# Performance work log

Measured on AMD Instinct MI355X. Metric: run time of the kernel, lower is better.

The kernel has to match this reference:

```python
import jax, jax.numpy as jnp
import numpy as np

N, IN_F, H, D = 3072, 512, 8, 64


def setup_inputs() -> dict:
    key = jax.random.key(0)
    k1, k2, k3, k4, k5 = jax.random.split(key, 5)
    x = jax.random.normal(k1, (N, IN_F), dtype=jnp.float32)
    adj = jax.random.randint(k2, (N, N), 0, 2, dtype=jnp.int32)
    # xavier-uniform-like scales
    s_W = (6.0 / (IN_F + H * D)) ** 0.5
    s_a = (6.0 / (H + D)) ** 0.5
    W = jax.random.uniform(k3, (H * D, IN_F), dtype=jnp.float32, minval=-s_W, maxval=s_W)
    a_src = jax.random.uniform(k4, (H, D), dtype=jnp.float32, minval=-s_a, maxval=s_a)
    a_dst = jax.random.uniform(k5, (H, D), dtype=jnp.float32, minval=-s_a, maxval=s_a)
    return {"x": x, "adj": adj, "W": W, "a_src": a_src, "a_dst": a_dst}


def reference(x, adj, W, a_src, a_dst):
    n = x.shape[0]
    Hh, d = a_src.shape
    h = (x @ W.T).reshape(n, Hh, d)                      # [n, H, d]
    e_src = jnp.einsum('nhd,hd->nh', h, a_src)           # [n, H]
    e_dst = jnp.einsum('nhd,hd->nh', h, a_dst)           # [n, H]
    e = e_src[:, None, :] + e_dst[None, :, :]            # [n, n, H], e[i,j]=src_i+dst_j
    e = jax.nn.leaky_relu(e, negative_slope=0.2)
    mask = (adj + jnp.eye(n, dtype=adj.dtype)) > 0       # [n, n]
    e = jnp.where(mask[:, :, None], e, -jnp.inf)
    alpha = jax.nn.softmax(e, axis=1)                    # softmax over j (neighbors)
    # out[i,h,d] = sum_j alpha[i,j,h] * h[j,h,d]  (dropout=0 / eval mode)
    out = jnp.einsum('ijh,jhd->ihd', alpha, h)
    return out.reshape(n, Hh * d)                        # concat=True
```

## Files before the change

### kernel.cpp

```cpp
#include <hip/hip_runtime.h>
#include <hip/hip_bf16.h>

typedef __bf16 bf16x8 __attribute__((ext_vector_type(8)));
typedef _Float16 half8 __attribute__((ext_vector_type(8)));
typedef _Float16 half2v __attribute__((ext_vector_type(2)));
typedef short s16x2 __attribute__((ext_vector_type(2)));
typedef float f32x4 __attribute__((ext_vector_type(4)));
typedef float f32x16 __attribute__((ext_vector_type(16)));

#define NROW 3072
#define NF 512
#define NH 8
#define ND 64
#define GEMM_BLOCKS 384

__device__ __forceinline__ unsigned gat_enc_key(float f) {
    unsigned u = __float_as_uint(f);
    return (f < 0.f) ? ~u : (u | 0x80000000u);
}
__device__ __forceinline__ float gat_dec_key(unsigned k) {
    unsigned u = (k & 0x80000000u) ? (k ^ 0x80000000u) : ~k;
    return __uint_as_float(u);
}

__device__ __forceinline__ bf16x8 gat_ld_cvt8(const float* p) {
    float4 f0 = *reinterpret_cast<const float4*>(p);
    float4 f1 = *reinterpret_cast<const float4*>(p + 4);
    bf16x8 o = { (__bf16)f0.x, (__bf16)f0.y, (__bf16)f0.z, (__bf16)f0.w,
                 (__bf16)f1.x, (__bf16)f1.y, (__bf16)f1.z, (__bf16)f1.w };
    return o;
}

__global__ __launch_bounds__(256) void gat_gemm_bp(const float* __restrict__ x,
                                                   const float* __restrict__ W,
                                                   _Float16* __restrict__ hT,
                                                   const int* __restrict__ adj,
                                                   unsigned long long* __restrict__ bits64,
                                                   const float* __restrict__ a_src,
                                                   const float* __restrict__ a_dst,
                                                   float* __restrict__ e_srcT,
                                                   float* __restrict__ e_dstT,
                                                   unsigned* __restrict__ maxkey) {
    __shared__ __align__(16) __bf16 sA[2][4096];
    __shared__ __align__(16) __bf16 sB[2][4096];
    __shared__ float ered[2][2][2][32];

    if (blockIdx.x >= GEMM_BLOCKS) {
        int i = blockIdx.x - GEMM_BLOCKS;
        int wave = threadIdx.x >> 6;
        int lane = threadIdx.x & 63;
        const int* row = adj + i * NROW;
#pragma unroll
        for (int it = 0; it < 12; ++it) {
            int base = wave * 768 + it * 64;
            int j = base + lane;
            bool pred = (row[j] > 0) || (j == i);
            unsigned long long bal = __ballot(pred);
            if (lane == 0) bits64[i * 48 + (base >> 6)] = bal;
        }
        return;
    }

    int b = blockIdx.x;
    int i0 = (b >> 3) * 64;
    int o0 = (b & 7) * 64;
    int head = b & 7;
    int tid = threadIdx.x;
    int wave = tid >> 6;
    int lane = tid & 63;
    int half = lane >> 5;
    int l31 = lane & 31;
    int wr = wave >> 1;
    int wc = wave & 1;

    int v0 = tid, v1 = tid + 256;
    int r0 = v0 >> 3, r1 = v1 >> 3;
    int cc0 = ((v0 & 7) ^ (r0 & 7)) << 3;
    int cc1 = ((v1 & 7) ^ (r1 & 7)) << 3;
    const float* gA0 = x + (i0 + r0) * NF + cc0;
    const float* gA1 = x + (i0 + r1) * NF + cc1;
    const float* gB0 = W + (o0 + r0) * NF + cc0;
    const float* gB1 = W + (o0 + r1) * NF + cc1;

    *reinterpret_cast<bf16x8*>(&sA[0][v0 * 8]) = gat_ld_cvt8(gA0);
    *reinterpret_cast<bf16x8*>(&sA[0][v1 * 8]) = gat_ld_cvt8(gA1);
    *reinterpret_cast<bf16x8*>(&sB[0][v0 * 8]) = gat_ld_cvt8(gB0);
    *reinterpret_cast<bf16x8*>(&sB[0][v1 * 8]) = gat_ld_cvt8(gB1);
    __syncthreads();

    f32x16 acc = {};
    int arow = (wr * 32 + l31) * 64;
    int brow = (wc * 32 + l31) * 64;
    int sw7 = l31 & 7;

    for (int c = 0; c < 8; ++c) {
        bf16x8 na0, na1, nb0, nb1;
        bool more = (c < 7);
        if (more) {
            na0 = gat_ld_cvt8(gA0 + (c + 1) * 64);
            na1 = gat_ld_cvt8(gA1 + (c + 1) * 64);
            nb0 = gat_ld_cvt8(gB0 + (c + 1) * 64);
            nb1 = gat_ld_cvt8(gB1 + (c + 1) * 64);
        }
        const __bf16* pa = &sA[c & 1][0];
        const __bf16* pb = &sB[c & 1][0];
#pragma unroll
        for (int ks = 0; ks < 4; ++ks) {
            int q = (((ks << 1) | half) ^ sw7) << 3;
            bf16x8 a = *reinterpret_cast<const bf16x8*>(pa + arow + q);
            bf16x8 bb = *reinterpret_cast<const bf16x8*>(pb + brow + q);
            acc = __builtin_amdgcn_mfma_f32_32x32x16_bf16(a, bb, acc, 0, 0, 0);
        }
        if (more) {
            *reinterpret_cast<bf16x8*>(&sA[(c + 1) & 1][v0 * 8]) = na0;
            *reinterpret_cast<bf16x8*>(&sA[(c + 1) & 1][v1 * 8]) = na1;
            *reinterpret_cast<bf16x8*>(&sB[(c + 1) & 1][v0 * 8]) = nb0;
            *reinterpret_cast<bf16x8*>(&sB[(c + 1) & 1][v1 * 8]) = nb1;
        }
        __syncthreads();
    }

    _Float16* tt = reinterpret_cast<_Float16*>(&sA[0][0]) + wave * 1280;
#pragma unroll
    for (int reg = 0; reg < 16; ++reg) {
        int rowl = (reg & 3) + 8 * (reg >> 2) + 4 * half;
        tt[rowl * 40 + l31] = (_Float16)acc[reg];
    }
    int orow = lane >> 1;
    int li = (lane & 1) * 16;
    half8 h0, h1;
#pragma unroll
    for (int t = 0; t < 8; ++t) h0[t] = tt[(li + t) * 40 + orow];
#pragma unroll
    for (int t = 0; t < 8; ++t) h1[t] = tt[(li + 8 + t) * 40 + orow];
    _Float16* op = hT + (long)(o0 + wc * 32 + orow) * NROW + i0 + wr * 32 + li;
    *reinterpret_cast<half8*>(op) = h0;
    *reinterpret_cast<half8*>(op + 8) = h1;

    half8 hv0 = *reinterpret_cast<const half8*>(tt + l31 * 40 + half * 16);
    half8 hv1 = *reinterpret_cast<const half8*>(tt + l31 * 40 + half * 16 + 8);
    const float* ap = a_src + head * ND + wc * 32 + half * 16;
    const float* dp = a_dst + head * ND + wc * 32 + half * 16;
    float4 as0 = *reinterpret_cast<const float4*>(ap);
    float4 as1 = *reinterpret_cast<const float4*>(ap + 4);
    float4 as2 = *reinterpret_cast<const float4*>(ap + 8);
    float4 as3 = *reinterpret_cast<const float4*>(ap + 12);
    float4 ad0 = *reinterpret_cast<const float4*>(dp);
    float4 ad1 = *reinterpret_cast<const float4*>(dp + 4);
    float4 ad2 = *reinterpret_cast<const float4*>(dp + 8);
    float4 ad3 = *reinterpret_cast<const float4*>(dp + 12);
    float ps = 0.f, pd = 0.f;
    ps += (float)hv0[0]*as0.x + (float)hv0[1]*as0.y + (float)hv0[2]*as0.z + (float)hv0[3]*as0.w;
    ps += (float)hv0[4]*as1.x + (float)hv0[5]*as1.y + (float)hv0[6]*as1.z + (float)hv0[7]*as1.w;
    ps += (float)hv1[0]*as2.x + (float)hv1[1]*as2.y + (float)hv1[2]*as2.z + (float)hv1[3]*as2.w;
    ps += (float)hv1[4]*as3.x + (float)hv1[5]*as3.y + (float)hv1[6]*as3.z + (float)hv1[7]*as3.w;
    pd += (float)hv0[0]*ad0.x + (float)hv0[1]*ad0.y + (float)hv0[2]*ad0.z + (float)hv0[3]*ad0.w;
    pd += (float)hv0[4]*ad1.x + (float)hv0[5]*ad1.y + (float)hv0[6]*ad1.z + (float)hv0[7]*ad1.w;
    pd += (float)hv1[0]*ad2.x + (float)hv1[1]*ad2.y + (float)hv1[2]*ad2.z + (float)hv1[3]*ad2.w;
    pd += (float)hv1[4]*ad3.x + (float)hv1[5]*ad3.y + (float)hv1[6]*ad3.z + (float)hv1[7]*ad3.w;
    ps += __shfl_xor(ps, 32, 64);
    pd += __shfl_xor(pd, 32, 64);
    if (half == 0) { ered[0][wr][wc][l31] = ps; ered[1][wr][wc][l31] = pd; }
    __syncthreads();
    if (wc == 0) {
        float pst = ered[0][wr][0][l31] + ered[0][wr][1][l31];
        float pdt = ered[1][wr][0][l31] + ered[1][wr][1][l31];
        if (half == 0) {
            e_srcT[head * NROW + i0 + wr * 32 + l31] = pst;
            e_dstT[head * NROW + i0 + wr * 32 + l31] = pdt;
        }
        float mx = pdt;
#pragma unroll
        for (int off = 1; off < 32; off <<= 1) mx = fmaxf(mx, __shfl_xor(mx, off, 64));
        if (lane == 0) atomicMax(&maxkey[head], gat_enc_key(mx));
    }
}

__global__ __launch_bounds__(256) void gat_attn(const unsigned* __restrict__ bits,
                                                const float* __restrict__ e_srcT,
                                                const float* __restrict__ e_dstT,
                                                const unsigned* __restrict__ maxkey,
                                                const _Float16* __restrict__ hT,
                                                _Float16* __restrict__ num,
                                                float* __restrict__ den) {
    constexpr int JCHUNK = NROW / 4;
    constexpr int NC = JCHUNK / 64;
    __shared__ unsigned lds_P[JCHUNK / 2];
    __shared__ unsigned lds_Q[JCHUNK / 2];
    __shared__ __align__(16) _Float16 hbuf[2][4096];
    int b = blockIdx.x;
    int head = b & 7;
    int jc = (b >> 3) & 3;
    int i0 = ((b >> 3) >> 2) * 128;
    int jbase = jc * JCHUNK;
    int tid = threadIdx.x;
    int wave = tid >> 6;
    int lane = tid & 63;
    int half = lane >> 5;
    int l31 = lane & 31;

    float Mg = gat_dec_key(maxkey[head]);
    for (int p = tid; p < JCHUNK / 2; p += 256) {
        float t0 = e_dstT[head * NROW + jbase + 2 * p] - Mg;
        float t1 = e_dstT[head * NROW + jbase + 2 * p + 1] - Mg;
        half2v P = { (_Float16)__expf(t0), (_Float16)__expf(t1) };
        half2v Q = { (_Float16)__expf(0.2f * t0), (_Float16)__expf(0.2f * t1) };
        lds_P[p] = __builtin_bit_cast(unsigned, P);
        lds_Q[p] = __builtin_bit_cast(unsigned, Q);
    }

    int irow = i0 + wave * 32 + l31;
    float u = e_srcT[head * NROW + irow] + Mg;
    float Rf = fminf(__expf(-0.8f * u), 60000.f);
    _Float16 Rh = (_Float16)Rf;
    half2v R2 = { Rh, Rh };
    const half8 ones8 = { (_Float16)1.f, (_Float16)1.f, (_Float16)1.f, (_Float16)1.f,
                          (_Float16)1.f, (_Float16)1.f, (_Float16)1.f, (_Float16)1.f };
    const unsigned* brow = bits + irow * 96 + jc * (JCHUNK / 32);

    int s0 = tid, s1 = tid + 256;
    const _Float16* gp0 = hT + (head * ND + ((s0 >> 6) & 1) * 32 + (s0 & 31)) * NROW
                             + jbase + (s0 >> 7) * 16 + ((s0 >> 5) & 1) * 8;
    const _Float16* gp1 = hT + (head * ND + ((s1 >> 6) & 1) * 32 + (s1 & 31)) * NROW
                             + jbase + (s1 >> 7) * 16 + ((s1 >> 5) & 1) * 8;
    *reinterpret_cast<half8*>(&hbuf[0][tid * 8])         = *reinterpret_cast<const half8*>(gp0);
    *reinterpret_cast<half8*>(&hbuf[0][(tid + 256) * 8]) = *reinterpret_cast<const half8*>(gp1);
    __syncthreads();

    f32x16 acc0 = {};
    f32x16 acc1 = {};
    f32x16 acc2 = {};
    uint2 wm = *reinterpret_cast<const uint2*>(brow);

    for (int k = 0; k < NC; ++k) {
        half8 st0, st1;
        uint2 wmn = wm;
        bool more = (k + 1 < NC);
        if (more) {
            st0 = *reinterpret_cast<const half8*>(gp0 + (k + 1) * 64);
            st1 = *reinterpret_cast<const half8*>(gp1 + (k + 1) * 64);
            wmn = *reinterpret_cast<const uint2*>(brow + (k + 1) * 2);
        }
        const _Float16* hb = &hbuf[k & 1][0];
#pragma unroll
        for (int js = 0; js < 4; ++js) {
            unsigned word = (js < 2) ? wm.x : wm.y;
            unsigned w8 = (word >> ((js & 1) * 16 + half * 8)) & 0xffu;
            unsigned long long S64 = ((unsigned long long)(w8 & 0x55u) << 15)
                                   | ((unsigned long long)(w8 & 0xAAu) << 30);
            uint4 Pv = *reinterpret_cast<const uint4*>(&lds_P[k * 32 + js * 8 + half * 4]);
            uint4 Qv = *reinterpret_cast<const uint4*>(&lds_Q[k * 32 + js * 8 + half * 4]);
            unsigned pr[4] = { Pv.x, Pv.y, Pv.z, Pv.w };
            unsigned qr[4] = { Qv.x, Qv.y, Qv.z, Qv.w };
            unsigned am[4];
#pragma unroll
            for (int t = 0; t < 4; ++t) {
                half2v qq = __builtin_bit_cast(half2v, qr[t]) * R2;
                half2v mx = __builtin_elementwise_max(
                                __builtin_bit_cast(half2v, pr[t]), qq);
                unsigned Wt = (unsigned)(S64 >> (2 * t));
                s16x2 mks = __builtin_bit_cast(s16x2, Wt) >> 15;
                am[t] = __builtin_bit_cast(unsigned, mx)
                      & __builtin_bit_cast(unsigned, mks);
            }
            uint4 m4 = { am[0], am[1], am[2], am[3] };
            half8 af = __builtin_bit_cast(half8, m4);
            half8 v0 = *reinterpret_cast<const half8*>(hb + (js * 128 + lane) * 8);
            half8 v1 = *reinterpret_cast<const half8*>(hb + (js * 128 + 64 + lane) * 8);
            acc0 = __builtin_amdgcn_mfma_f32_32x32x16_f16(af, v0, acc0, 0, 0, 0);
            acc1 = __builtin_amdgcn_mfma_f32_32x32x16_f16(af, v1, acc1, 0, 0, 0);
            acc2 = __builtin_amdgcn_mfma_f32_32x32x16_f16(af, ones8, acc2, 0, 0, 0);
        }
        if (more) {
            *reinterpret_cast<half8*>(&hbuf[(k + 1) & 1][tid * 8])         = st0;
            *reinterpret_cast<half8*>(&hbuf[(k + 1) & 1][(tid + 256) * 8]) = st1;
        }
        wm = wmn;
        __syncthreads();
    }

#pragma unroll
    for (int reg = 0; reg < 16; ++reg) {
        int rowl = (reg & 3) + 8 * (reg >> 2) + 4 * half;
        if (l31 == 0)
            den[(long)(jc * NROW + i0 + wave * 32 + rowl) * NH + head] = acc2[reg];
        long ob = (long)(jc * NROW + i0 + wave * 32 + rowl) * NF + head * ND + l31;
        num[ob]      = (_Float16)acc0[reg];
        num[ob + 32] = (_Float16)acc1[reg];
    }
}

__global__ __launch_bounds__(256) void gat_final(const _Float16* __restrict__ num,
                                                 const float* __restrict__ den,
                                                 float* __restrict__ out) {
    int idx = (blockIdx.x * 256 + threadIdx.x) * 8;
    int i = idx >> 9;
    int c = idx & 511;
    int head = c >> 6;
    half8 n0 = *reinterpret_cast<const half8*>(num + (long)i * NF + c);
    half8 n1 = *reinterpret_cast<const half8*>(num + (long)(NROW + i) * NF + c);
    half8 n2 = *reinterpret_cast<const half8*>(num + (long)(2 * NROW + i) * NF + c);
    half8 n3 = *reinterpret_cast<const half8*>(num + (long)(3 * NROW + i) * NF + c);
    float ds = den[i * NH + head] + den[(NROW + i) * NH + head]
             + den[(2 * NROW + i) * NH + head] + den[(3 * NROW + i) * NH + head];
    float inv = 1.0f / fmaxf(ds, 1e-30f);
    float r0 = ((float)n0[0] + (float)n1[0] + (float)n2[0] + (float)n3[0]) * inv;
    float r1 = ((float)n0[1] + (float)n1[1] + (float)n2[1] + (float)n3[1]) * inv;
    float r2 = ((float)n0[2] + (float)n1[2] + (float)n2[2] + (float)n3[2]) * inv;
    float r3 = ((float)n0[3] + (float)n1[3] + (float)n2[3] + (float)n3[3]) * inv;
    float r4 = ((float)n0[4] + (float)n1[4] + (float)n2[4] + (float)n3[4]) * inv;
    float r5 = ((float)n0[5] + (float)n1[5] + (float)n2[5] + (float)n3[5]) * inv;
    float r6 = ((float)n0[6] + (float)n1[6] + (float)n2[6] + (float)n3[6]) * inv;
    float r7 = ((float)n0[7] + (float)n1[7] + (float)n2[7] + (float)n3[7]) * inv;
    float4 o0 = { r0, r1, r2, r3 };
    float4 o1 = { r4, r5, r6, r7 };
    *reinterpret_cast<float4*>(out + idx)     = o0;
    *reinterpret_cast<float4*>(out + idx + 4) = o1;
}

extern "C" void kernel_launch(void* const* d_in, const int* in_sizes, int n_in,
                              void* d_out, int out_size, void* d_ws, size_t ws_size,
                              hipStream_t stream) {
    const float* x_raw  = (const float*)d_in[0];
    const int*   adj    = (const int*)d_in[1];
    const float* W_raw  = (const float*)d_in[2];
    const float* as_raw = (const float*)d_in[3];
    const float* ad_raw = (const float*)d_in[4];
    float* out = (float*)d_out;

    char* ws = (char*)d_ws;
    _Float16* hT     = (_Float16*)(ws);
    float*    e_srcT = (float*)(ws + 3145728);
    float*    e_dstT = (float*)(ws + 3244032);
    unsigned* maxkey = (unsigned*)(ws + 3342336);
    unsigned* bits   = (unsigned*)(ws + 3342400);
    _Float16* num    = (_Float16*)(ws + 8192064);
    float*    den    = (float*)(ws + 20774976);

    hipMemsetAsync(maxkey, 0, 64, stream);
    gat_gemm_bp<<<GEMM_BLOCKS + NROW, 256, 0, stream>>>(x_raw, W_raw, hT, adj,
                                                        (unsigned long long*)bits,
                                                        as_raw, ad_raw,
                                                        e_srcT, e_dstT, maxkey);
    gat_attn<<<24 * 4 * 8, 256, 0, stream>>>(bits, e_srcT, e_dstT, maxkey, hT, num, den);
    gat_final<<<NROW * NF / 2048, 256, 0, stream>>>(num, den, out);
}
```

Baseline: 143.3 us.

## Pack adjacency bits with vectorized int4 loads and shrink GEMM K-tile to 32

The adjacency bitmask pass now has each thread read 32 ints with int4 loads and build one 32-bit word, replacing per-element wave ballots over 3072 blocks with 1152 denser blocks. Bit order stays the same, so downstream consumers are unaffected. The projection GEMM switches from a 64-wide XOR-swizzled K tile to a 32-wide padded (stride 40) tile with 16 stages, which lowers shared memory use and per-thread loads. In exchange the GEMM pays more barriers per block.

```diff
diff --git a/kernel.cpp b/kernel.cpp
--- a/kernel.cpp
+++ b/kernel.cpp
@@ -13,6 +13,7 @@
 #define NH 8
 #define ND 64
 #define GEMM_BLOCKS 384
+#define BP_BLOCKS 1152
 
 __device__ __forceinline__ unsigned gat_enc_key(float f) {
     unsigned u = __float_as_uint(f);
@@ -35,29 +36,33 @@
                                                    const float* __restrict__ W,
                                                    _Float16* __restrict__ hT,
                                                    const int* __restrict__ adj,
-                                                   unsigned long long* __restrict__ bits64,
+                                                   unsigned* __restrict__ bits,
                                                    const float* __restrict__ a_src,
                                                    const float* __restrict__ a_dst,
                                                    float* __restrict__ e_srcT,
                                                    float* __restrict__ e_dstT,
                                                    unsigned* __restrict__ maxkey) {
-    __shared__ __align__(16) __bf16 sA[2][4096];
-    __shared__ __align__(16) __bf16 sB[2][4096];
+    __shared__ __align__(16) _Float16 smem[10240];
     __shared__ float ered[2][2][2][32];
 
     if (blockIdx.x >= GEMM_BLOCKS) {
-        int i = blockIdx.x - GEMM_BLOCKS;
-        int wave = threadIdx.x >> 6;
-        int lane = threadIdx.x & 63;
-        const int* row = adj + i * NROW;
-#pragma unroll
-        for (int it = 0; it < 12; ++it) {
-            int base = wave * 768 + it * 64;
-            int j = base + lane;
-            bool pred = (row[j] > 0) || (j == i);
-            unsigned long long bal = __ballot(pred);
-            if (lane == 0) bits64[i * 48 + (base >> 6)] = bal;
-        }
+        int g = (blockIdx.x - GEMM_BLOCKS) * 256 + threadIdx.x;
+        int row = g / 96;
+        int seg = g - row * 96;
+        const int* p = adj + row * NROW + seg * 32;
+        unsigned w = 0;
+#pragma unroll
+        for (int q = 0; q < 8; ++q) {
+            int4 v = *reinterpret_cast<const int4*>(p + q * 4);
+            unsigned b0 = (v.x > 0) ? 1u : 0u;
+            unsigned b1 = (v.y > 0) ? 2u : 0u;
+            unsigned b2 = (v.z > 0) ? 4u : 0u;
+            unsigned b3 = (v.w > 0) ? 8u : 0u;
+            w |= (b0 | b1 | b2 | b3) << (q * 4);
+        }
+        int d = row - seg * 32;
+        if ((unsigned)d < 32u) w |= 1u << d;
+        bits[g] = w;
         return;
     }
 
@@ -73,54 +78,47 @@
     int wr = wave >> 1;
     int wc = wave & 1;
 
-    int v0 = tid, v1 = tid + 256;
-    int r0 = v0 >> 3, r1 = v1 >> 3;
-    int cc0 = ((v0 & 7) ^ (r0 & 7)) << 3;
-    int cc1 = ((v1 & 7) ^ (r1 & 7)) << 3;
-    const float* gA0 = x + (i0 + r0) * NF + cc0;
-    const float* gA1 = x + (i0 + r1) * NF + cc1;
-    const float* gB0 = W + (o0 + r0) * NF + cc0;
-    const float* gB1 = W + (o0 + r1) * NF + cc1;
-
-    *reinterpret_cast<bf16x8*>(&sA[0][v0 * 8]) = gat_ld_cvt8(gA0);
-    *reinterpret_cast<bf16x8*>(&sA[0][v1 * 8]) = gat_ld_cvt8(gA1);
-    *reinterpret_cast<bf16x8*>(&sB[0][v0 * 8]) = gat_ld_cvt8(gB0);
-    *reinterpret_cast<bf16x8*>(&sB[0][v1 * 8]) = gat_ld_cvt8(gB1);
+    __bf16* sA = reinterpret_cast<__bf16*>(smem);
+    __bf16* sB = reinterpret_cast<__bf16*>(smem) + 5120;
+
+    int r = tid >> 2;
+    int pp = tid & 3;
+    const float* gA = x + (i0 + r) * NF + pp * 8;
+    const float* gB = W + (o0 + r) * NF + pp * 8;
+    int dslot = r * 40 + pp * 8;
+
+    *reinterpret_cast<bf16x8*>(sA + dslot) = gat_ld_cvt8(gA);
+    *reinterpret_cast<bf16x8*>(sB + dslot) = gat_ld_cvt8(gB);
     __syncthreads();
 
     f32x16 acc = {};
-    int arow = (wr * 32 + l31) * 64;
-    int brow = (wc * 32 + l31) * 64;
-    int sw7 = l31 & 7;
-
-    for (int c = 0; c < 8; ++c) {
-        bf16x8 na0, na1, nb0, nb1;
-        bool more = (c < 7);
+    int arow = (wr * 32 + l31) * 40;
+    int brow = (wc * 32 + l31) * 40;
+
+    for (int c = 0; c < 16; ++c) {
+        bf16x8 na, nb;
+        bool more = (c < 15);
         if (more) {
-            na0 = gat_ld_cvt8(gA0 + (c + 1) * 64);
-            na1 = gat_ld_cvt8(gA1 + (c + 1) * 64);
-            nb0 = gat_ld_cvt8(gB0 + (c + 1) * 64);
-            nb1 = gat_ld_cvt8(gB1 + (c + 1) * 64);
-        }
-        const __bf16* pa = &sA[c & 1][0];
-        const __bf16* pb = &sB[c & 1][0];
-#pragma unroll
-        for (int ks = 0; ks < 4; ++ks) {
-            int q = (((ks << 1) | half) ^ sw7) << 3;
+            na = gat_ld_cvt8(gA + (c + 1) * 32);
+            nb = gat_ld_cvt8(gB + (c + 1) * 32);
+        }
+        const __bf16* pa = sA + (c & 1) * 2560;
+        const __bf16* pb = sB + (c & 1) * 2560;
+#pragma unroll
+        for (int ks = 0; ks < 2; ++ks) {
+            int q = (((ks << 1) | half)) << 3;
             bf16x8 a = *reinterpret_cast<const bf16x8*>(pa + arow + q);
             bf16x8 bb = *reinterpret_cast<const bf16x8*>(pb + brow + q);
             acc = __builtin_amdgcn_mfma_f32_32x32x16_bf16(a, bb, acc, 0, 0, 0);
         }
         if (more) {
-            *reinterpret_cast<bf16x8*>(&sA[(c + 1) & 1][v0 * 8]) = na0;
-            *reinterpret_cast<bf16x8*>(&sA[(c + 1) & 1][v1 * 8]) = na1;
-            *reinterpret_cast<bf16x8*>(&sB[(c + 1) & 1][v0 * 8]) = nb0;
-            *reinterpret_cast<bf16x8*>(&sB[(c + 1) & 1][v1 * 8]) = nb1;
+            *reinterpret_cast<bf16x8*>(sA + ((c + 1) & 1) * 2560 + dslot) = na;
+            *reinterpret_cast<bf16x8*>(sB + ((c + 1) & 1) * 2560 + dslot) = nb;
         }
         __syncthreads();
     }
 
-    _Float16* tt = reinterpret_cast<_Float16*>(&sA[0][0]) + wave * 1280;
+    _Float16* tt = smem + wave * 1280;
 #pragma unroll
     for (int reg = 0; reg < 16; ++reg) {
         int rowl = (reg & 3) + 8 * (reg >> 2) + 4 * half;
@@ -338,10 +336,9 @@
     float*    den    = (float*)(ws + 20774976);
 
     hipMemsetAsync(maxkey, 0, 64, stream);
-    gat_gemm_bp<<<GEMM_BLOCKS + NROW, 256, 0, stream>>>(x_raw, W_raw, hT, adj,
-                                                        (unsigned long long*)bits,
-                                                        as_raw, ad_raw,
-                                                        e_srcT, e_dstT, maxkey);
+    gat_gemm_bp<<<GEMM_BLOCKS + BP_BLOCKS, 256, 0, stream>>>(x_raw, W_raw, hT, adj,
+                                                             bits, as_raw, ad_raw,
+                                                             e_srcT, e_dstT, maxkey);
     gat_attn<<<24 * 4 * 8, 256, 0, stream>>>(bits, e_srcT, e_dstT, maxkey, hT, num, den);
     gat_final<<<NROW * NF / 2048, 256, 0, stream>>>(num, den, out);
 }
```

After: 135.2 us. 5.6% less time.
